# Performance work log

Measured on AMD Instinct MI355X. Metric: run time of the kernel, lower is better.

The kernel has to match this reference:

```python
import jax, jax.numpy as jnp
import numpy as np

N_NODES = 10000
N_EDGES = 320000
N_GRAPHS = 64
IN_DIM = 1
HID = 256


def setup_inputs() -> dict:
    key = jax.random.key(0)
    ks = jax.random.split(key, 12)
    s = 1.0 / np.sqrt(HID)
    inp = {
        "x": jax.random.normal(ks[0], (N_NODES, IN_DIM), dtype=jnp.float32),
        "edge_index": jax.random.randint(ks[1], (2, N_EDGES), 0, N_NODES, dtype=jnp.int64),
        "batch": jnp.sort(jax.random.randint(ks[2], (N_NODES,), 0, N_GRAPHS, dtype=jnp.int64)),
        "W_emb": jax.random.normal(ks[3], (IN_DIM, HID), dtype=jnp.float32),
        "b_emb": jnp.zeros((HID,), dtype=jnp.float32),
        "W1a": jax.random.normal(ks[4], (HID, HID), dtype=jnp.float32) * s,
        "b1a": jnp.zeros((HID,), dtype=jnp.float32),
        "W1b": jax.random.normal(ks[5], (HID, HID), dtype=jnp.float32) * s,
        "b1b": jnp.zeros((HID,), dtype=jnp.float32),
        "W2a": jax.random.normal(ks[6], (HID, HID), dtype=jnp.float32) * s,
        "b2a": jnp.zeros((HID,), dtype=jnp.float32),
        "W2b": jax.random.normal(ks[7], (HID, HID), dtype=jnp.float32) * s,
        "b2b": jnp.zeros((HID,), dtype=jnp.float32),
    }
    return inp


def _pointnet_conv(h, src, dst, Wa, ba, Wb, bb):
    # gather x_j -> 2-layer MLP per edge -> scatter-max at dst (PyG aggr='max')
    msg = jax.nn.relu(h[src] @ Wa + ba) @ Wb + bb          # [E, HID]
    agg = jax.ops.segment_max(msg, dst, num_segments=N_NODES)
    # PyG fills nodes with no incoming messages with 0
    return jnp.where(jnp.isneginf(agg), 0.0, agg)


def reference(x, edge_index, batch, W_emb, b_emb, W1a, b1a, W1b, b1b, W2a, b2a, W2b, b2b):
    src, dst = edge_index[0], edge_index[1]
    h = jax.nn.silu(x @ W_emb + b_emb)                     # [N, HID]
    h = h + jax.nn.silu(_pointnet_conv(h, src, dst, W1a, b1a, W1b, b1b))
    h = h + jax.nn.silu(_pointnet_conv(h, src, dst, W2a, b2a, W2b, b2b))
    # global_mean_pool over graphs
    sums = jax.ops.segment_sum(h, batch, num_segments=N_GRAPHS)          # [G, HID]
    cnts = jax.ops.segment_sum(jnp.ones((h.shape[0],), h.dtype), batch, num_segments=N_GRAPHS)
    return sums / jnp.maximum(cnts, 1.0)[:, None]
```

## Files before the change

kernel.cpp:

```cpp
#include <hip/hip_runtime.h>
#include <hip/hip_bf16.h>
#include <math.h>

#define HID 256
#define CAP 128

typedef __attribute__((ext_vector_type(8))) short bf16x8;
typedef __attribute__((ext_vector_type(8))) unsigned short u16x8;
typedef __attribute__((ext_vector_type(4))) float f32x4;

__device__ __forceinline__ float silu_f(float z) {
    return z / (1.0f + __expf(-z));
}
__device__ __forceinline__ unsigned short f2bf(float f) {
    unsigned int u = __float_as_uint(f);
    u = (u + 0x7FFFu + ((u >> 16) & 1u)) >> 16;
    return (unsigned short)u;
}
__device__ __forceinline__ float bf2f(unsigned short b) {
    return __uint_as_float(((unsigned int)b) << 16);
}
__device__ __forceinline__ void max8(float m[8], u16x8 v) {
#pragma unroll
    for (int k = 0; k < 8; ++k) m[k] = fmaxf(m[k], bf2f(v[k]));
}

__global__ __launch_bounds__(256) void k_prep(
    const float* __restrict__ w0, const float* __restrict__ w1,
    const float* __restrict__ w2, const float* __restrict__ w3,
    unsigned short* __restrict__ o0, unsigned short* __restrict__ o1,
    unsigned short* __restrict__ o2, unsigned short* __restrict__ o3,
    const int* __restrict__ src, const int* __restrict__ dst,
    int* __restrict__ cnt, int* __restrict__ csr,
    const int* __restrict__ batch, int* __restrict__ goff,
    int N, int E, int G, int nh) {
    __shared__ float ls[64][65];
    int b = blockIdx.x;
    int tid = threadIdx.x;
    if (b < 64) {
        int mat = b >> 4;
        int tile = b & 15;
        int k0 = (tile >> 2) * 64;
        int n0 = (tile & 3) * 64;
        const float* in = (mat == 0) ? w0 : (mat == 1) ? w1 : (mat == 2) ? w2 : w3;
        unsigned short* op = (mat == 0) ? o0 : (mat == 1) ? o1 : (mat == 2) ? o2 : o3;
        int lrb = tid >> 4;
        int lc = (tid & 15) * 4;
#pragma unroll
        for (int p = 0; p < 4; ++p) {
            int lr = p * 16 + lrb;
            float4 v = *(const float4*)(in + (size_t)(k0 + lr) * HID + n0 + lc);
            ls[lr][lc + 0] = v.x; ls[lr][lc + 1] = v.y;
            ls[lr][lc + 2] = v.z; ls[lr][lc + 3] = v.w;
        }
        __syncthreads();
#pragma unroll
        for (int p = 0; p < 4; ++p) {
            int ln = p * 16 + lrb;
            ushort4 q;
            q.x = f2bf(ls[lc + 0][ln]);
            q.y = f2bf(ls[lc + 1][ln]);
            q.z = f2bf(ls[lc + 2][ln]);
            q.w = f2bf(ls[lc + 3][ln]);
            *(ushort4*)(op + (size_t)(n0 + ln) * HID + k0 + lc) = q;
        }
    } else if (b < 64 + nh) {
        int e = (b - 64) * 256 + tid;
        if (e < E) {
            int d = dst[e];
            int p = atomicAdd(&cnt[d], 1);
            if (p < CAP) csr[d * CAP + p] = src[e];
        }
    } else {
        int g = tid;
        if (g > G) return;
        int lo = 0, hi = N;
        while (lo < hi) {
            int mid = (lo + hi) >> 1;
            if (batch[mid] < g) lo = mid + 1; else hi = mid;
        }
        goff[g] = lo;
    }
}

template <bool FIRST>
__global__ __launch_bounds__(256) void k_mlp(
    const float* __restrict__ x, const float* __restrict__ Wemb,
    const float* __restrict__ bemb, const unsigned short* __restrict__ Aglob,
    const unsigned short* __restrict__ Wta, const float* __restrict__ ba,
    const unsigned short* __restrict__ Wtb, const float* __restrict__ bbv,
    unsigned short* __restrict__ hb, unsigned short* __restrict__ t2, int M) {
    __shared__ unsigned short As[FIRST ? 32 : 1][264];
    __shared__ unsigned short t1s[32][264];
    int tid = threadIdx.x;
    int lane = tid & 63;
    int wave = tid >> 6;
    int quad = lane >> 4;
    int r = lane & 15;
    int m0 = blockIdx.x * 32;
    int colw = wave * 64;

    if (FIRST) {
        int row = tid >> 3;
        int c0 = (tid & 7) * 32;
        int grow = m0 + row;
        float xv = (grow < M) ? x[grow] : 0.0f;
#pragma unroll
        for (int j = 0; j < 8; ++j) {
            int c = c0 + j * 4;
            ushort4 q;
            q.x = f2bf(silu_f(xv * Wemb[c + 0] + bemb[c + 0]));
            q.y = f2bf(silu_f(xv * Wemb[c + 1] + bemb[c + 1]));
            q.z = f2bf(silu_f(xv * Wemb[c + 2] + bemb[c + 2]));
            q.w = f2bf(silu_f(xv * Wemb[c + 3] + bemb[c + 3]));
            if (grow < M) *(ushort4*)(hb + (size_t)grow * HID + c) = q;
            *(ushort4*)&As[row][c] = q;
        }
        __syncthreads();
    }

    f32x4 acc[2][4];
#pragma unroll
    for (int rt = 0; rt < 2; ++rt)
#pragma unroll
        for (int nt = 0; nt < 4; ++nt) acc[rt][nt] = (f32x4)0.0f;

    int ar0 = m0 + r;        if (ar0 >= M) ar0 = M - 1;
    int ar1 = m0 + 16 + r;   if (ar1 >= M) ar1 = M - 1;

#pragma unroll
    for (int ks = 0; ks < 8; ++ks) {
        bf16x8 a0, a1;
        if (FIRST) {
            a0 = *(const bf16x8*)&As[r][ks * 32 + quad * 8];
            a1 = *(const bf16x8*)&As[(FIRST ? r + 16 : 0)][ks * 32 + quad * 8];
        } else {
            a0 = *(const bf16x8*)(Aglob + (size_t)ar0 * HID + ks * 32 + quad * 8);
            a1 = *(const bf16x8*)(Aglob + (size_t)ar1 * HID + ks * 32 + quad * 8);
        }
#pragma unroll
        for (int nt = 0; nt < 4; ++nt) {
            bf16x8 bfr = *(const bf16x8*)(Wta + (size_t)(colw + nt * 16 + r) * HID
                                          + ks * 32 + quad * 8);
            acc[0][nt] = __builtin_amdgcn_mfma_f32_16x16x32_bf16(a0, bfr, acc[0][nt], 0, 0, 0);
            acc[1][nt] = __builtin_amdgcn_mfma_f32_16x16x32_bf16(a1, bfr, acc[1][nt], 0, 0, 0);
        }
    }

#pragma unroll
    for (int nt = 0; nt < 4; ++nt) {
        int col = colw + nt * 16 + r;
        float bv = ba[col];
#pragma unroll
        for (int rt = 0; rt < 2; ++rt)
#pragma unroll
            for (int i = 0; i < 4; ++i) {
                float v = fmaxf(acc[rt][nt][i] + bv, 0.0f);
                t1s[rt * 16 + quad * 4 + i][col] = f2bf(v);
            }
    }
    __syncthreads();

    f32x4 acc2[2][4];
#pragma unroll
    for (int rt = 0; rt < 2; ++rt)
#pragma unroll
        for (int nt = 0; nt < 4; ++nt) acc2[rt][nt] = (f32x4)0.0f;
#pragma unroll
    for (int ks = 0; ks < 8; ++ks) {
        bf16x8 a0 = *(const bf16x8*)&t1s[r][ks * 32 + quad * 8];
        bf16x8 a1 = *(const bf16x8*)&t1s[r + 16][ks * 32 + quad * 8];
#pragma unroll
        for (int nt = 0; nt < 4; ++nt) {
            bf16x8 bfr = *(const bf16x8*)(Wtb + (size_t)(colw + nt * 16 + r) * HID
                                          + ks * 32 + quad * 8);
            acc2[0][nt] = __builtin_amdgcn_mfma_f32_16x16x32_bf16(a0, bfr, acc2[0][nt], 0, 0, 0);
            acc2[1][nt] = __builtin_amdgcn_mfma_f32_16x16x32_bf16(a1, bfr, acc2[1][nt], 0, 0, 0);
        }
    }

#pragma unroll
    for (int nt = 0; nt < 4; ++nt) {
        int col = colw + nt * 16 + r;
        float bv = bbv[col];
#pragma unroll
        for (int rt = 0; rt < 2; ++rt)
#pragma unroll
            for (int i = 0; i < 4; ++i) {
                int row = m0 + rt * 16 + quad * 4 + i;
                if (row < M) t2[(size_t)row * HID + col] = f2bf(acc2[rt][nt][i] + bv);
            }
    }
}

__global__ __launch_bounds__(256) void k_agg(const unsigned short* __restrict__ t2,
                                             const int* __restrict__ cnt,
                                             const int* __restrict__ csr,
                                             unsigned short* __restrict__ hb, int N) {
    int lane = threadIdx.x & 63;
    int node = (blockIdx.x * blockDim.x + threadIdx.x) >> 6;
    if (node >= N) return;
    int half = lane >> 5;
    int lc = (lane & 31) * 8;
    const unsigned short* base = t2 + lc;

    int deg = cnt[node];
    if (deg > CAP) deg = CAP;
    const int* rowp = csr + (size_t)node * CAP;
    size_t o = (size_t)node * HID + lc;
    u16x8 hq = *(const u16x8*)(hb + o);

    float m[8];
#pragma unroll
    for (int k = 0; k < 8; ++k) m[k] = -INFINITY;

    int i = 0;
    for (; i + 16 <= deg; i += 16) {
        int s[8];
#pragma unroll
        for (int j = 0; j < 8; ++j) s[j] = rowp[i + 2 * j + half];
        u16x8 v[8];
#pragma unroll
        for (int j = 0; j < 8; ++j) v[j] = *(const u16x8*)(base + (size_t)s[j] * HID);
#pragma unroll
        for (int j = 0; j < 8; ++j) max8(m, v[j]);
    }
    if (i + 8 <= deg) {
        int s[4];
#pragma unroll
        for (int j = 0; j < 4; ++j) s[j] = rowp[i + 2 * j + half];
        u16x8 v[4];
#pragma unroll
        for (int j = 0; j < 4; ++j) v[j] = *(const u16x8*)(base + (size_t)s[j] * HID);
#pragma unroll
        for (int j = 0; j < 4; ++j) max8(m, v[j]);
        i += 8;
    }
    for (; i < deg; i += 2) {
        int idx = i + half; if (idx >= deg) idx = deg - 1;
        int s = rowp[idx];
        u16x8 v = *(const u16x8*)(base + (size_t)s * HID);
        max8(m, v);
    }

#pragma unroll
    for (int k = 0; k < 8; ++k) m[k] = fmaxf(m[k], __shfl_xor(m[k], 32, 64));
    if (deg == 0) {
#pragma unroll
        for (int k = 0; k < 8; ++k) m[k] = 0.0f;
    }

    if (half == 0) {
        u16x8 q;
#pragma unroll
        for (int k = 0; k < 8; ++k) q[k] = f2bf(bf2f(hq[k]) + silu_f(m[k]));
        *(u16x8*)(hb + o) = q;
    }
}

__global__ __launch_bounds__(1024) void k_pool(const unsigned short* __restrict__ hb,
                                               const int* __restrict__ goff,
                                               float* __restrict__ out) {
    __shared__ float part[3][HID];
    int g = blockIdx.x;
    int tid = threadIdx.x;
    int c = tid & 255;
    int chunk = tid >> 8;
    int beg = goff[g], end = goff[g + 1];
    float s = 0.f;
    for (int n = beg + chunk; n < end; n += 4) s += bf2f(hb[(size_t)n * HID + c]);
    if (chunk > 0) part[chunk - 1][c] = s;
    __syncthreads();
    if (chunk == 0) {
        s += part[0][c] + part[1][c] + part[2][c];
        int cnt = end - beg;
        out[g * HID + c] = s / (float)(cnt > 0 ? cnt : 1);
    }
}

extern "C" void kernel_launch(void* const* d_in, const int* in_sizes, int n_in,
                              void* d_out, int out_size, void* d_ws, size_t ws_size,
                              hipStream_t stream) {
    const float* x     = (const float*)d_in[0];
    const int*   ei    = (const int*)d_in[1];
    const int*   batch = (const int*)d_in[2];
    const float* Wemb  = (const float*)d_in[3];
    const float* bemb  = (const float*)d_in[4];
    const float* W1a   = (const float*)d_in[5];
    const float* b1a   = (const float*)d_in[6];
    const float* W1b   = (const float*)d_in[7];
    const float* b1b   = (const float*)d_in[8];
    const float* W2a   = (const float*)d_in[9];
    const float* b2a   = (const float*)d_in[10];
    const float* W2b   = (const float*)d_in[11];
    const float* b2b   = (const float*)d_in[12];
    float* out = (float*)d_out;

    const int N = in_sizes[0];
    const int E = in_sizes[1] / 2;
    const int G = out_size / HID;
    const int* src = ei;
    const int* dst = ei + E;

    char* ws = (char*)d_ws;
    unsigned short* hb   = (unsigned short*)ws; ws += (size_t)N * HID * 2;
    unsigned short* t2   = (unsigned short*)ws; ws += (size_t)N * HID * 2;
    unsigned short* Wt1a = (unsigned short*)ws; ws += (size_t)HID * HID * 2;
    unsigned short* Wt1b = (unsigned short*)ws; ws += (size_t)HID * HID * 2;
    unsigned short* Wt2a = (unsigned short*)ws; ws += (size_t)HID * HID * 2;
    unsigned short* Wt2b = (unsigned short*)ws; ws += (size_t)HID * HID * 2;
    int* cnt  = (int*)ws; ws += (size_t)N * 4;
    int* goff = (int*)ws; ws += (size_t)(G + 1) * 4;
    int* csr  = (int*)ws; ws += (size_t)N * CAP * 4;

    const int nh = (E + 255) / 256;

    hipMemsetAsync(cnt, 0, (size_t)N * 4, stream);

    k_prep<<<64 + nh + 1, 256, 0, stream>>>(W1a, W1b, W2a, W2b,
                                            Wt1a, Wt1b, Wt2a, Wt2b,
                                            src, dst, cnt, csr,
                                            batch, goff, N, E, G, nh);

    dim3 mgrid((N + 31) / 32);
    int agg_blocks = (N * 64 + 255) / 256;

    k_mlp<true ><<<mgrid, 256, 0, stream>>>(x, Wemb, bemb, nullptr,
                                            Wt1a, b1a, Wt1b, b1b, hb, t2, N);
    k_agg<<<agg_blocks, 256, 0, stream>>>(t2, cnt, csr, hb, N);

    k_mlp<false><<<mgrid, 256, 0, stream>>>(nullptr, nullptr, nullptr, hb,
                                            Wt2a, b2a, Wt2b, b2b, hb, t2, N);
    k_agg<<<agg_blocks, 256, 0, stream>>>(t2, cnt, csr, hb, N);

    k_pool<<<G, 1024, 0, stream>>>(hb, goff, out);
}
```

Baseline: 207.0 us.

## Fuse all stages into one persistent cooperative kernel with grid syncs

Replaces the memset and the five separate kernel launches with a single cooperative kernel of 512 blocks. Grid-wide barriers separate weight prep, the first MLP, aggregation, the second MLP, the second aggregation and pooling. The CSR edge bucketing now runs on the blocks left idle during the first MLP, so it overlaps that phase, and cnt zeroing moves inside the kernel. This removes launch gaps, but aggregation now runs with a fixed number of resident waves striding over nodes, which may hide less gather latency, and each grid sync adds cost.

After: 525.3 us. 2.54x slower.

```diff
diff --git a/kernel.cpp b/kernel.cpp
--- a/kernel.cpp
+++ b/kernel.cpp
@@ -1,9 +1,11 @@
 #include <hip/hip_runtime.h>
+#include <hip/hip_cooperative_groups.h>
 #include <hip/hip_bf16.h>
 #include <math.h>
 
 #define HID 256
 #define CAP 128
+#define NBLK 512
 
 typedef __attribute__((ext_vector_type(8))) short bf16x8;
 typedef __attribute__((ext_vector_type(8))) unsigned short u16x8;
@@ -25,79 +27,32 @@
     for (int k = 0; k < 8; ++k) m[k] = fmaxf(m[k], bf2f(v[k]));
 }
 
-__global__ __launch_bounds__(256) void k_prep(
-    const float* __restrict__ w0, const float* __restrict__ w1,
-    const float* __restrict__ w2, const float* __restrict__ w3,
-    unsigned short* __restrict__ o0, unsigned short* __restrict__ o1,
-    unsigned short* __restrict__ o2, unsigned short* __restrict__ o3,
-    const int* __restrict__ src, const int* __restrict__ dst,
-    int* __restrict__ cnt, int* __restrict__ csr,
-    const int* __restrict__ batch, int* __restrict__ goff,
-    int N, int E, int G, int nh) {
-    __shared__ float ls[64][65];
-    int b = blockIdx.x;
-    int tid = threadIdx.x;
-    if (b < 64) {
-        int mat = b >> 4;
-        int tile = b & 15;
-        int k0 = (tile >> 2) * 64;
-        int n0 = (tile & 3) * 64;
-        const float* in = (mat == 0) ? w0 : (mat == 1) ? w1 : (mat == 2) ? w2 : w3;
-        unsigned short* op = (mat == 0) ? o0 : (mat == 1) ? o1 : (mat == 2) ? o2 : o3;
-        int lrb = tid >> 4;
-        int lc = (tid & 15) * 4;
-#pragma unroll
-        for (int p = 0; p < 4; ++p) {
-            int lr = p * 16 + lrb;
-            float4 v = *(const float4*)(in + (size_t)(k0 + lr) * HID + n0 + lc);
-            ls[lr][lc + 0] = v.x; ls[lr][lc + 1] = v.y;
-            ls[lr][lc + 2] = v.z; ls[lr][lc + 3] = v.w;
-        }
-        __syncthreads();
-#pragma unroll
-        for (int p = 0; p < 4; ++p) {
-            int ln = p * 16 + lrb;
-            ushort4 q;
-            q.x = f2bf(ls[lc + 0][ln]);
-            q.y = f2bf(ls[lc + 1][ln]);
-            q.z = f2bf(ls[lc + 2][ln]);
-            q.w = f2bf(ls[lc + 3][ln]);
-            *(ushort4*)(op + (size_t)(n0 + ln) * HID + k0 + lc) = q;
-        }
-    } else if (b < 64 + nh) {
-        int e = (b - 64) * 256 + tid;
-        if (e < E) {
-            int d = dst[e];
-            int p = atomicAdd(&cnt[d], 1);
-            if (p < CAP) csr[d * CAP + p] = src[e];
-        }
-    } else {
-        int g = tid;
-        if (g > G) return;
-        int lo = 0, hi = N;
-        while (lo < hi) {
-            int mid = (lo + hi) >> 1;
-            if (batch[mid] < g) lo = mid + 1; else hi = mid;
-        }
-        goff[g] = lo;
-    }
-}
+struct Params {
+    const float* x;
+    const int* src; const int* dst; const int* batch;
+    const float* Wemb; const float* bemb;
+    const float* W1a; const float* b1a; const float* W1b; const float* b1b;
+    const float* W2a; const float* b2a; const float* W2b; const float* b2b;
+    float* out;
+    unsigned short* hb; unsigned short* t2;
+    unsigned short* Wt1a; unsigned short* Wt1b;
+    unsigned short* Wt2a; unsigned short* Wt2b;
+    int* cnt; int* csr; int* goff;
+    int N; int E; int G;
+};
 
 template <bool FIRST>
-__global__ __launch_bounds__(256) void k_mlp(
+__device__ __forceinline__ void mlp_tile(
+    int m0, int tid, unsigned short (*As)[264], unsigned short (*t1s)[264],
     const float* __restrict__ x, const float* __restrict__ Wemb,
     const float* __restrict__ bemb, const unsigned short* __restrict__ Aglob,
     const unsigned short* __restrict__ Wta, const float* __restrict__ ba,
     const unsigned short* __restrict__ Wtb, const float* __restrict__ bbv,
     unsigned short* __restrict__ hb, unsigned short* __restrict__ t2, int M) {
-    __shared__ unsigned short As[FIRST ? 32 : 1][264];
-    __shared__ unsigned short t1s[32][264];
-    int tid = threadIdx.x;
     int lane = tid & 63;
     int wave = tid >> 6;
     int quad = lane >> 4;
     int r = lane & 15;
-    int m0 = blockIdx.x * 32;
     int colw = wave * 64;
 
     if (FIRST) {
@@ -133,7 +88,7 @@
         bf16x8 a0, a1;
         if (FIRST) {
             a0 = *(const bf16x8*)&As[r][ks * 32 + quad * 8];
-            a1 = *(const bf16x8*)&As[(FIRST ? r + 16 : 0)][ks * 32 + quad * 8];
+            a1 = *(const bf16x8*)&As[r + 16][ks * 32 + quad * 8];
         } else {
             a0 = *(const bf16x8*)(Aglob + (size_t)ar0 * HID + ks * 32 + quad * 8);
             a1 = *(const bf16x8*)(Aglob + (size_t)ar1 * HID + ks * 32 + quad * 8);
@@ -178,7 +133,6 @@
             acc2[1][nt] = __builtin_amdgcn_mfma_f32_16x16x32_bf16(a1, bfr, acc2[1][nt], 0, 0, 0);
         }
     }
-
 #pragma unroll
     for (int nt = 0; nt < 4; ++nt) {
         int col = colw + nt * 16 + r;
@@ -193,17 +147,14 @@
     }
 }
 
-__global__ __launch_bounds__(256) void k_agg(const unsigned short* __restrict__ t2,
-                                             const int* __restrict__ cnt,
-                                             const int* __restrict__ csr,
-                                             unsigned short* __restrict__ hb, int N) {
-    int lane = threadIdx.x & 63;
-    int node = (blockIdx.x * blockDim.x + threadIdx.x) >> 6;
-    if (node >= N) return;
+__device__ __forceinline__ void agg_node(int node, int lane,
+                                         const unsigned short* __restrict__ t2,
+                                         const int* __restrict__ cnt,
+                                         const int* __restrict__ csr,
+                                         unsigned short* __restrict__ hb) {
     int half = lane >> 5;
     int lc = (lane & 31) * 8;
     const unsigned short* base = t2 + lc;
-
     int deg = cnt[node];
     if (deg > CAP) deg = CAP;
     const int* rowp = csr + (size_t)node * CAP;
@@ -249,7 +200,6 @@
 #pragma unroll
         for (int k = 0; k < 8; ++k) m[k] = 0.0f;
     }
-
     if (half == 0) {
         u16x8 q;
 #pragma unroll
@@ -258,49 +208,119 @@
     }
 }
 
-__global__ __launch_bounds__(1024) void k_pool(const unsigned short* __restrict__ hb,
-                                               const int* __restrict__ goff,
-                                               float* __restrict__ out) {
-    __shared__ float part[3][HID];
-    int g = blockIdx.x;
+__global__ __launch_bounds__(256, 2) void k_all(Params p) {
+    namespace cg = cooperative_groups;
+    cg::grid_group grid = cg::this_grid();
+    __shared__ unsigned char smem[33792];
+    unsigned short (*As)[264]  = (unsigned short(*)[264])smem;
+    unsigned short (*t1s)[264] = (unsigned short(*)[264])(smem + 16896);
+    int b = blockIdx.x;
     int tid = threadIdx.x;
-    int c = tid & 255;
-    int chunk = tid >> 8;
-    int beg = goff[g], end = goff[g + 1];
-    float s = 0.f;
-    for (int n = beg + chunk; n < end; n += 4) s += bf2f(hb[(size_t)n * HID + c]);
-    if (chunk > 0) part[chunk - 1][c] = s;
-    __syncthreads();
-    if (chunk == 0) {
-        s += part[0][c] + part[1][c] + part[2][c];
-        int cnt = end - beg;
-        out[g * HID + c] = s / (float)(cnt > 0 ? cnt : 1);
+    int lane = tid & 63;
+    int wave = tid >> 6;
+    int MT = (p.N + 31) / 32;
+
+    if (b < 64) {
+        float (*ls)[65] = (float(*)[65])smem;
+        int mat = b >> 4;
+        int tile = b & 15;
+        int k0 = (tile >> 2) * 64;
+        int n0 = (tile & 3) * 64;
+        const float* in = (mat == 0) ? p.W1a : (mat == 1) ? p.W1b
+                        : (mat == 2) ? p.W2a : p.W2b;
+        unsigned short* op = (mat == 0) ? p.Wt1a : (mat == 1) ? p.Wt1b
+                           : (mat == 2) ? p.Wt2a : p.Wt2b;
+        int lrb = tid >> 4;
+        int lc = (tid & 15) * 4;
+#pragma unroll
+        for (int q = 0; q < 4; ++q) {
+            int lr = q * 16 + lrb;
+            float4 v = *(const float4*)(in + (size_t)(k0 + lr) * HID + n0 + lc);
+            ls[lr][lc + 0] = v.x; ls[lr][lc + 1] = v.y;
+            ls[lr][lc + 2] = v.z; ls[lr][lc + 3] = v.w;
+        }
+        __syncthreads();
+#pragma unroll
+        for (int q = 0; q < 4; ++q) {
+            int ln = q * 16 + lrb;
+            ushort4 w;
+            w.x = f2bf(ls[lc + 0][ln]);
+            w.y = f2bf(ls[lc + 1][ln]);
+            w.z = f2bf(ls[lc + 2][ln]);
+            w.w = f2bf(ls[lc + 3][ln]);
+            *(ushort4*)(op + (size_t)(n0 + ln) * HID + k0 + lc) = w;
+        }
+    } else if (b == 64) {
+        if (tid <= p.G) {
+            int lo = 0, hi = p.N;
+            while (lo < hi) {
+                int mid = (lo + hi) >> 1;
+                if (p.batch[mid] < tid) lo = mid + 1; else hi = mid;
+            }
+            p.goff[tid] = lo;
+        }
+    } else {
+        int i = (b - 65) * 256 + tid;
+        if (i < p.N) p.cnt[i] = 0;
+    }
+    grid.sync();
+
+    if (b < MT) {
+        mlp_tile<true>(b * 32, tid, As, t1s, p.x, p.Wemb, p.bemb, nullptr,
+                       p.Wt1a, p.b1a, p.Wt1b, p.b1b, p.hb, p.t2, p.N);
+    } else {
+        int nb = NBLK - MT;
+        for (int e = (b - MT) * 256 + tid; e < p.E; e += nb * 256) {
+            int d = p.dst[e];
+            int q = atomicAdd(&p.cnt[d], 1);
+            if (q < CAP) p.csr[d * CAP + q] = p.src[e];
+        }
+    }
+    grid.sync();
+
+    {
+        const int TOTW = NBLK * 4;
+        for (int node = b * 4 + wave; node < p.N; node += TOTW)
+            agg_node(node, lane, p.t2, p.cnt, p.csr, p.hb);
+    }
+    grid.sync();
+
+    if (b < MT) {
+        mlp_tile<false>(b * 32, tid, As, t1s, nullptr, nullptr, nullptr, p.hb,
+                        p.Wt2a, p.b2a, p.Wt2b, p.b2b, p.hb, p.t2, p.N);
+    }
+    grid.sync();
+
+    {
+        const int TOTW = NBLK * 4;
+        for (int node = b * 4 + wave; node < p.N; node += TOTW)
+            agg_node(node, lane, p.t2, p.cnt, p.csr, p.hb);
+    }
+    grid.sync();
+
+    if (b < p.G) {
+        int g = b, c = tid;
+        int beg = p.goff[g], end = p.goff[g + 1];
+        float s = 0.f;
+        int n = beg;
+        for (; n + 4 <= end; n += 4) {
+            s += bf2f(p.hb[(size_t)(n + 0) * HID + c])
+               + bf2f(p.hb[(size_t)(n + 1) * HID + c])
+               + bf2f(p.hb[(size_t)(n + 2) * HID + c])
+               + bf2f(p.hb[(size_t)(n + 3) * HID + c]);
+        }
+        for (; n < end; ++n) s += bf2f(p.hb[(size_t)n * HID + c]);
+        int cg_ = end - beg;
+        p.out[g * HID + c] = s / (float)(cg_ > 0 ? cg_ : 1);
     }
 }
 
 extern "C" void kernel_launch(void* const* d_in, const int* in_sizes, int n_in,
                               void* d_out, int out_size, void* d_ws, size_t ws_size,
                               hipStream_t stream) {
-    const float* x     = (const float*)d_in[0];
-    const int*   ei    = (const int*)d_in[1];
-    const int*   batch = (const int*)d_in[2];
-    const float* Wemb  = (const float*)d_in[3];
-    const float* bemb  = (const float*)d_in[4];
-    const float* W1a   = (const float*)d_in[5];
-    const float* b1a   = (const float*)d_in[6];
-    const float* W1b   = (const float*)d_in[7];
-    const float* b1b   = (const float*)d_in[8];
-    const float* W2a   = (const float*)d_in[9];
-    const float* b2a   = (const float*)d_in[10];
-    const float* W2b   = (const float*)d_in[11];
-    const float* b2b   = (const float*)d_in[12];
-    float* out = (float*)d_out;
-
     const int N = in_sizes[0];
     const int E = in_sizes[1] / 2;
     const int G = out_size / HID;
-    const int* src = ei;
-    const int* dst = ei + E;
 
     char* ws = (char*)d_ws;
     unsigned short* hb   = (unsigned short*)ws; ws += (size_t)N * HID * 2;
@@ -313,25 +333,28 @@
     int* goff = (int*)ws; ws += (size_t)(G + 1) * 4;
     int* csr  = (int*)ws; ws += (size_t)N * CAP * 4;
 
-    const int nh = (E + 255) / 256;
-
-    hipMemsetAsync(cnt, 0, (size_t)N * 4, stream);
-
-    k_prep<<<64 + nh + 1, 256, 0, stream>>>(W1a, W1b, W2a, W2b,
-                                            Wt1a, Wt1b, Wt2a, Wt2b,
-                                            src, dst, cnt, csr,
-                                            batch, goff, N, E, G, nh);
-
-    dim3 mgrid((N + 31) / 32);
-    int agg_blocks = (N * 64 + 255) / 256;
-
-    k_mlp<true ><<<mgrid, 256, 0, stream>>>(x, Wemb, bemb, nullptr,
-                                            Wt1a, b1a, Wt1b, b1b, hb, t2, N);
-    k_agg<<<agg_blocks, 256, 0, stream>>>(t2, cnt, csr, hb, N);
-
-    k_mlp<false><<<mgrid, 256, 0, stream>>>(nullptr, nullptr, nullptr, hb,
-                                            Wt2a, b2a, Wt2b, b2b, hb, t2, N);
-    k_agg<<<agg_blocks, 256, 0, stream>>>(t2, cnt, csr, hb, N);
-
-    k_pool<<<G, 1024, 0, stream>>>(hb, goff, out);
-}
+    Params p;
+    p.x     = (const float*)d_in[0];
+    p.src   = (const int*)d_in[1];
+    p.dst   = (const int*)d_in[1] + E;
+    p.batch = (const int*)d_in[2];
+    p.Wemb  = (const float*)d_in[3];
+    p.bemb  = (const float*)d_in[4];
+    p.W1a   = (const float*)d_in[5];
+    p.b1a   = (const float*)d_in[6];
+    p.W1b   = (const float*)d_in[7];
+    p.b1b   = (const float*)d_in[8];
+    p.W2a   = (const float*)d_in[9];
+    p.b2a   = (const float*)d_in[10];
+    p.W2b   = (const float*)d_in[11];
+    p.b2b   = (const float*)d_in[12];
+    p.out   = (float*)d_out;
+    p.hb = hb; p.t2 = t2;
+    p.Wt1a = Wt1a; p.Wt1b = Wt1b; p.Wt2a = Wt2a; p.Wt2b = Wt2b;
+    p.cnt = cnt; p.csr = csr; p.goff = goff;
+    p.N = N; p.E = E; p.G = G;
+
+    void* args[] = { &p };
+    hipLaunchCooperativeKernel((const void*)k_all, dim3(NBLK), dim3(256),
+                               args, 0, stream);
+}
```

## Split aggregation per node across two waves by column half, four edges per wave

Applied to the files above, without the earlier changes.

The max-aggregation kernel now launches two wavefronts per node, each covering half of the 256 feature columns. Inside a wave, four groups of 16 lanes each handle a different edge, so more edges are in flight at once and the gather loop runs fewer iterations. The intent is more memory-level parallelism and shorter per-node latency for the irregular gather. The cost is twice as many waves, an extra cross-lane shuffle step, more redundant index loads, and each lane group now reads 256-byte segments instead of 512-byte ones.

Result: no change. 209.4 us (+1.2%).

```diff
diff --git a/kernel.cpp b/kernel.cpp
--- a/kernel.cpp
+++ b/kernel.cpp
@@ -197,60 +197,77 @@
                                              const int* __restrict__ cnt,
                                              const int* __restrict__ csr,
                                              unsigned short* __restrict__ hb, int N) {
+    int gw = (blockIdx.x * blockDim.x + threadIdx.x) >> 6;
     int lane = threadIdx.x & 63;
-    int node = (blockIdx.x * blockDim.x + threadIdx.x) >> 6;
+    int half = (gw >= N) ? 1 : 0;
+    int node = gw - half * N;
     if (node >= N) return;
-    int half = lane >> 5;
-    int lc = (lane & 31) * 8;
+    int quad = lane >> 4;
+    int li = lane & 15;
+    int lc = half * 128 + li * 8;
     const unsigned short* base = t2 + lc;
 
     int deg = cnt[node];
     if (deg > CAP) deg = CAP;
     const int* rowp = csr + (size_t)node * CAP;
     size_t o = (size_t)node * HID + lc;
-    u16x8 hq = *(const u16x8*)(hb + o);
+    u16x8 hq;
+    if (quad == 0) hq = *(const u16x8*)(hb + o);
 
     float m[8];
 #pragma unroll
     for (int k = 0; k < 8; ++k) m[k] = -INFINITY;
 
     int i = 0;
-    for (; i + 16 <= deg; i += 16) {
+    for (; i + 32 <= deg; i += 32) {
         int s[8];
 #pragma unroll
-        for (int j = 0; j < 8; ++j) s[j] = rowp[i + 2 * j + half];
+        for (int j = 0; j < 8; ++j) s[j] = rowp[i + 4 * j + quad];
         u16x8 v[8];
 #pragma unroll
         for (int j = 0; j < 8; ++j) v[j] = *(const u16x8*)(base + (size_t)s[j] * HID);
 #pragma unroll
         for (int j = 0; j < 8; ++j) max8(m, v[j]);
     }
+    if (i + 16 <= deg) {
+        int s[4];
+#pragma unroll
+        for (int j = 0; j < 4; ++j) s[j] = rowp[i + 4 * j + quad];
+        u16x8 v[4];
+#pragma unroll
+        for (int j = 0; j < 4; ++j) v[j] = *(const u16x8*)(base + (size_t)s[j] * HID);
+#pragma unroll
+        for (int j = 0; j < 4; ++j) max8(m, v[j]);
+        i += 16;
+    }
     if (i + 8 <= deg) {
-        int s[4];
-#pragma unroll
-        for (int j = 0; j < 4; ++j) s[j] = rowp[i + 2 * j + half];
-        u16x8 v[4];
-#pragma unroll
-        for (int j = 0; j < 4; ++j) v[j] = *(const u16x8*)(base + (size_t)s[j] * HID);
-#pragma unroll
-        for (int j = 0; j < 4; ++j) max8(m, v[j]);
+        int s[2];
+#pragma unroll
+        for (int j = 0; j < 2; ++j) s[j] = rowp[i + 4 * j + quad];
+        u16x8 v[2];
+#pragma unroll
+        for (int j = 0; j < 2; ++j) v[j] = *(const u16x8*)(base + (size_t)s[j] * HID);
+#pragma unroll
+        for (int j = 0; j < 2; ++j) max8(m, v[j]);
         i += 8;
     }
-    for (; i < deg; i += 2) {
-        int idx = i + half; if (idx >= deg) idx = deg - 1;
+    for (; i < deg; i += 4) {
+        int idx = i + quad; if (idx >= deg) idx = deg - 1;
         int s = rowp[idx];
         u16x8 v = *(const u16x8*)(base + (size_t)s * HID);
         max8(m, v);
     }
 
 #pragma unroll
+    for (int k = 0; k < 8; ++k) m[k] = fmaxf(m[k], __shfl_xor(m[k], 16, 64));
+#pragma unroll
     for (int k = 0; k < 8; ++k) m[k] = fmaxf(m[k], __shfl_xor(m[k], 32, 64));
     if (deg == 0) {
 #pragma unroll
         for (int k = 0; k < 8; ++k) m[k] = 0.0f;
     }
 
-    if (half == 0) {
+    if (quad == 0) {
         u16x8 q;
 #pragma unroll
         for (int k = 0; k < 8; ++k) q[k] = f2bf(bf2f(hq[k]) + silu_f(m[k]));
@@ -323,7 +340,7 @@
                                             batch, goff, N, E, G, nh);
 
     dim3 mgrid((N + 31) / 32);
-    int agg_blocks = (N * 64 + 255) / 256;
+    int agg_blocks = (2 * N * 64 + 255) / 256;
 
     k_mlp<true ><<<mgrid, 256, 0, stream>>>(x, Wemb, bemb, nullptr,
                                             Wt1a, b1a, Wt1b, b1b, hb, t2, N);
```

## Move CSR build into first MLP kernel and zero counts in prep kernel

Applied to the files above, without the earlier changes.

The hipMemsetAsync of the in-degree counters is replaced by extra blocks in the prep kernel that zero them. The edge-bucketing (atomic CSR build) moves out of the prep kernel and runs as extra blocks of the first MLP launch, so it overlaps with the layer-1 GEMM work. The FIRST/not-FIRST template is split into two separate kernels. This saves one memset launch and aims to hide the atomic scatter behind compute, but it mixes two block types with different resource profiles (the MLP blocks use LDS) in one launch, which can affect occupancy.

Result: faster. 202.5 us (-2.2%).

```diff
diff --git a/kernel.cpp b/kernel.cpp
--- a/kernel.cpp
+++ b/kernel.cpp
@@ -30,10 +30,9 @@
     const float* __restrict__ w2, const float* __restrict__ w3,
     unsigned short* __restrict__ o0, unsigned short* __restrict__ o1,
     unsigned short* __restrict__ o2, unsigned short* __restrict__ o3,
-    const int* __restrict__ src, const int* __restrict__ dst,
-    int* __restrict__ cnt, int* __restrict__ csr,
+    int* __restrict__ cnt,
     const int* __restrict__ batch, int* __restrict__ goff,
-    int N, int E, int G, int nh) {
+    int N, int G) {
     __shared__ float ls[64][65];
     int b = blockIdx.x;
     int tid = threadIdx.x;
@@ -64,14 +63,7 @@
             q.w = f2bf(ls[lc + 3][ln]);
             *(ushort4*)(op + (size_t)(n0 + ln) * HID + k0 + lc) = q;
         }
-    } else if (b < 64 + nh) {
-        int e = (b - 64) * 256 + tid;
-        if (e < E) {
-            int d = dst[e];
-            int p = atomicAdd(&cnt[d], 1);
-            if (p < CAP) csr[d * CAP + p] = src[e];
-        }
-    } else {
+    } else if (b == 64) {
         int g = tid;
         if (g > G) return;
         int lo = 0, hi = N;
@@ -80,27 +72,44 @@
             if (batch[mid] < g) lo = mid + 1; else hi = mid;
         }
         goff[g] = lo;
-    }
-}
-
-template <bool FIRST>
-__global__ __launch_bounds__(256) void k_mlp(
+    } else {
+        int i = (b - 65) * 256 + tid;
+        if (i < N) cnt[i] = 0;
+    }
+}
+
+__global__ __launch_bounds__(256) void k_mlp1f(
     const float* __restrict__ x, const float* __restrict__ Wemb,
-    const float* __restrict__ bemb, const unsigned short* __restrict__ Aglob,
+    const float* __restrict__ bemb,
     const unsigned short* __restrict__ Wta, const float* __restrict__ ba,
     const unsigned short* __restrict__ Wtb, const float* __restrict__ bbv,
-    unsigned short* __restrict__ hb, unsigned short* __restrict__ t2, int M) {
-    __shared__ unsigned short As[FIRST ? 32 : 1][264];
+    unsigned short* __restrict__ hb, unsigned short* __restrict__ t2,
+    const int* __restrict__ src, const int* __restrict__ dst,
+    int* __restrict__ cnt, int* __restrict__ csr,
+    int M, int E, int MT) {
+    __shared__ unsigned short As[32][264];
     __shared__ unsigned short t1s[32][264];
+    int b = blockIdx.x;
     int tid = threadIdx.x;
+
+    if (b >= MT) {
+        int e = (b - MT) * 256 + tid;
+        if (e < E) {
+            int d = dst[e];
+            int p = atomicAdd(&cnt[d], 1);
+            if (p < CAP) csr[d * CAP + p] = src[e];
+        }
+        return;
+    }
+
     int lane = tid & 63;
     int wave = tid >> 6;
     int quad = lane >> 4;
     int r = lane & 15;
-    int m0 = blockIdx.x * 32;
+    int m0 = b * 32;
     int colw = wave * 64;
 
-    if (FIRST) {
+    {
         int row = tid >> 3;
         int c0 = (tid & 7) * 32;
         int grow = m0 + row;
@@ -124,20 +133,10 @@
     for (int rt = 0; rt < 2; ++rt)
 #pragma unroll
         for (int nt = 0; nt < 4; ++nt) acc[rt][nt] = (f32x4)0.0f;
-
-    int ar0 = m0 + r;        if (ar0 >= M) ar0 = M - 1;
-    int ar1 = m0 + 16 + r;   if (ar1 >= M) ar1 = M - 1;
-
 #pragma unroll
     for (int ks = 0; ks < 8; ++ks) {
-        bf16x8 a0, a1;
-        if (FIRST) {
-            a0 = *(const bf16x8*)&As[r][ks * 32 + quad * 8];
-            a1 = *(const bf16x8*)&As[(FIRST ? r + 16 : 0)][ks * 32 + quad * 8];
-        } else {
-            a0 = *(const bf16x8*)(Aglob + (size_t)ar0 * HID + ks * 32 + quad * 8);
-            a1 = *(const bf16x8*)(Aglob + (size_t)ar1 * HID + ks * 32 + quad * 8);
-        }
+        bf16x8 a0 = *(const bf16x8*)&As[r][ks * 32 + quad * 8];
+        bf16x8 a1 = *(const bf16x8*)&As[r + 16][ks * 32 + quad * 8];
 #pragma unroll
         for (int nt = 0; nt < 4; ++nt) {
             bf16x8 bfr = *(const bf16x8*)(Wta + (size_t)(colw + nt * 16 + r) * HID
@@ -146,7 +145,6 @@
             acc[1][nt] = __builtin_amdgcn_mfma_f32_16x16x32_bf16(a1, bfr, acc[1][nt], 0, 0, 0);
         }
     }
-
 #pragma unroll
     for (int nt = 0; nt < 4; ++nt) {
         int col = colw + nt * 16 + r;
@@ -178,7 +176,86 @@
             acc2[1][nt] = __builtin_amdgcn_mfma_f32_16x16x32_bf16(a1, bfr, acc2[1][nt], 0, 0, 0);
         }
     }
-
+#pragma unroll
+    for (int nt = 0; nt < 4; ++nt) {
+        int col = colw + nt * 16 + r;
+        float bv = bbv[col];
+#pragma unroll
+        for (int rt = 0; rt < 2; ++rt)
+#pragma unroll
+            for (int i = 0; i < 4; ++i) {
+                int row = m0 + rt * 16 + quad * 4 + i;
+                if (row < M) t2[(size_t)row * HID + col] = f2bf(acc2[rt][nt][i] + bv);
+            }
+    }
+}
+
+__global__ __launch_bounds__(256) void k_mlp2(
+    const unsigned short* __restrict__ Aglob,
+    const unsigned short* __restrict__ Wta, const float* __restrict__ ba,
+    const unsigned short* __restrict__ Wtb, const float* __restrict__ bbv,
+    unsigned short* __restrict__ t2, int M) {
+    __shared__ unsigned short t1s[32][264];
+    int tid = threadIdx.x;
+    int lane = tid & 63;
+    int wave = tid >> 6;
+    int quad = lane >> 4;
+    int r = lane & 15;
+    int m0 = blockIdx.x * 32;
+    int colw = wave * 64;
+
+    f32x4 acc[2][4];
+#pragma unroll
+    for (int rt = 0; rt < 2; ++rt)
+#pragma unroll
+        for (int nt = 0; nt < 4; ++nt) acc[rt][nt] = (f32x4)0.0f;
+
+    int ar0 = m0 + r;        if (ar0 >= M) ar0 = M - 1;
+    int ar1 = m0 + 16 + r;   if (ar1 >= M) ar1 = M - 1;
+
+#pragma unroll
+    for (int ks = 0; ks < 8; ++ks) {
+        bf16x8 a0 = *(const bf16x8*)(Aglob + (size_t)ar0 * HID + ks * 32 + quad * 8);
+        bf16x8 a1 = *(const bf16x8*)(Aglob + (size_t)ar1 * HID + ks * 32 + quad * 8);
+#pragma unroll
+        for (int nt = 0; nt < 4; ++nt) {
+            bf16x8 bfr = *(const bf16x8*)(Wta + (size_t)(colw + nt * 16 + r) * HID
+                                          + ks * 32 + quad * 8);
+            acc[0][nt] = __builtin_amdgcn_mfma_f32_16x16x32_bf16(a0, bfr, acc[0][nt], 0, 0, 0);
+            acc[1][nt] = __builtin_amdgcn_mfma_f32_16x16x32_bf16(a1, bfr, acc[1][nt], 0, 0, 0);
+        }
+    }
+#pragma unroll
+    for (int nt = 0; nt < 4; ++nt) {
+        int col = colw + nt * 16 + r;
+        float bv = ba[col];
+#pragma unroll
+        for (int rt = 0; rt < 2; ++rt)
+#pragma unroll
+            for (int i = 0; i < 4; ++i) {
+                float v = fmaxf(acc[rt][nt][i] + bv, 0.0f);
+                t1s[rt * 16 + quad * 4 + i][col] = f2bf(v);
+            }
+    }
+    __syncthreads();
+
+    f32x4 acc2[2][4];
+#pragma unroll
+    for (int rt = 0; rt < 2; ++rt)
+#pragma unroll
+        for (int nt = 0; nt < 4; ++nt) acc2[rt][nt] = (f32x4)0.0f;
+#pragma unroll
+    for (int ks = 0; ks < 8; ++ks) {
+        bf16x8 a0 = *(const bf16x8*)&t1s[r][ks * 32 + quad * 8];
+        bf16x8 a1 = *(const bf16x8*)&t1s[r + 16][ks * 32 + quad * 8];
+#pragma unroll
+        for (int nt = 0; nt < 4; ++nt) {
+            bf16x8 bfr = *(const bf16x8*)(Wtb + (size_t)(colw + nt * 16 + r) * HID
+                                          + ks * 32 + quad * 8);
+            acc2[0][nt] = __builtin_amdgcn_mfma_f32_16x16x32_bf16(a0, bfr, acc2[0][nt], 0, 0, 0);
+            acc2[1][nt] = __builtin_amdgcn_mfma_f32_16x16x32_bf16(a1, bfr, acc2[1][nt], 0, 0, 0);
+        }
+    }
 #pragma unroll
     for (int nt = 0; nt < 4; ++nt) {
         int col = colw + nt * 16 + r;
@@ -314,23 +391,22 @@
     int* csr  = (int*)ws; ws += (size_t)N * CAP * 4;
 
     const int nh = (E + 255) / 256;
-
-    hipMemsetAsync(cnt, 0, (size_t)N * 4, stream);
-
-    k_prep<<<64 + nh + 1, 256, 0, stream>>>(W1a, W1b, W2a, W2b,
+    const int nz = (N + 255) / 256;
+    const int MT = (N + 31) / 32;
+
+    k_prep<<<64 + 1 + nz, 256, 0, stream>>>(W1a, W1b, W2a, W2b,
                                             Wt1a, Wt1b, Wt2a, Wt2b,
-                                            src, dst, cnt, csr,
-                                            batch, goff, N, E, G, nh);
-
-    dim3 mgrid((N + 31) / 32);
+                                            cnt, batch, goff, N, G);
+
+    k_mlp1f<<<MT + nh, 256, 0, stream>>>(x, Wemb, bemb, Wt1a, b1a, Wt1b, b1b,
+                                         hb, t2, src, dst, cnt, csr, N, E, MT);
+
     int agg_blocks = (N * 64 + 255) / 256;
 
-    k_mlp<true ><<<mgrid, 256, 0, stream>>>(x, Wemb, bemb, nullptr,
-                                            Wt1a, b1a, Wt1b, b1b, hb, t2, N);
     k_agg<<<agg_blocks, 256, 0, stream>>>(t2, cnt, csr, hb, N);
 
-    k_mlp<false><<<mgrid, 256, 0, stream>>>(nullptr, nullptr, nullptr, hb,
-                                            Wt2a, b2a, Wt2b, b2b, hb, t2, N);
+    k_mlp2<<<MT, 256, 0, stream>>>(hb, Wt2a, b2a, Wt2b, b2b, t2, N);
+
     k_agg<<<agg_blocks, 256, 0, stream>>>(t2, cnt, csr, hb, N);
 
     k_pool<<<G, 1024, 0, stream>>>(hb, goff, out);
```
